# Kernel tuning notes

Hardware: AMD Instinct MI355X
Metric: run time of the kernel (lower is better)

## Reference

```python
import jax, jax.numpy as jnp
import numpy as np

B, T = 16, 512          # batch, timesteps
IN = 16                 # input_path_dim
D = 128                 # cde_state_dim
H = 256                 # vf_hidden_dim
L = 136                 # logsig_size = 16 + 16*15/2 (depth-2 log-signature)
O = 32                  # output_path_dim


def _linear_params(key, out_f, in_f):
    kw, kb = jax.random.split(key)
    lim = 1.0 / np.sqrt(in_f)
    W = jax.random.uniform(kw, (out_f, in_f), minval=-lim, maxval=lim, dtype=jnp.float32)
    b = jax.random.uniform(kb, (out_f,), minval=-lim, maxval=lim, dtype=jnp.float32)
    return W, b


def setup_inputs() -> dict:
    key = jax.random.key(0)
    ks = jax.random.split(key, 10)
    x0 = jax.random.normal(ks[0], (B, IN), dtype=jnp.float32)
    # log-signature increments are small; scale down for numerical realism
    logsigs = jax.random.normal(ks[1], (B, T - 1, L), dtype=jnp.float32) * 0.01
    # initial MLP: IN -> H -> H -> D (softplus activations, linear final)
    iw1, ib1 = _linear_params(ks[2], H, IN)
    iw2, ib2 = _linear_params(ks[3], H, H)
    iw3, ib3 = _linear_params(ks[4], D, H)
    # vector-field MLP: D -> H -> H -> D*L (softplus, tanh final)
    fw1, fb1 = _linear_params(ks[5], H, D)
    fw2, fb2 = _linear_params(ks[6], H, H)
    fw3, fb3 = _linear_params(ks[7], D * L, H)
    # readout: D -> O
    rw, rb = _linear_params(ks[8], O, D)
    return dict(x0=x0, logsigs=logsigs,
                iw1=iw1, ib1=ib1, iw2=iw2, ib2=ib2, iw3=iw3, ib3=ib3,
                fw1=fw1, fb1=fb1, fw2=fw2, fb2=fb2, fw3=fw3, fb3=fb3,
                rw=rw, rb=rb)


def reference(x0, logsigs, iw1, ib1, iw2, ib2, iw3, ib3,
              fw1, fb1, fw2, fb2, fw3, fb3, rw, rb):
    sp = jax.nn.softplus
    # initial MLP -> h0: (B, D)
    h0 = sp(x0 @ iw1.T + ib1)
    h0 = sp(h0 @ iw2.T + ib2)
    h0 = h0 @ iw3.T + ib3

    def step(h, logsig_t):
        # vector-field MLP: (B, D) -> (B, D*L), tanh final activation
        z = sp(h @ fw1.T + fb1)
        z = sp(z @ fw2.T + fb2)
        z = jnp.tanh(z @ fw3.T + fb3)
        mat = z.reshape(h.shape[0], D, L)          # (B, D, L)
        h_next = h + jnp.einsum('bdl,bl->bd', mat, logsig_t)
        return h_next, h_next

    # scan over time: xs shape (T-1, B, L)
    _, h_hist = jax.lax.scan(step, h0, jnp.swapaxes(logsigs, 0, 1))
    h_all = jnp.concatenate([h0[None, :, :], h_hist], axis=0)  # (T, B, D)
    out = h_all @ rw.T + rb                                     # (T, B, O)
    return jnp.swapaxes(out, 0, 1)                              # (B, T, O)
```

## Files before the change

kernel.cpp:

```cpp
#include <hip/hip_runtime.h>

namespace {
constexpr int kB = 16, kT = 512, kIN = 16, kD = 128, kH = 256, kL = 136, kO = 32;
constexpr int kSteps = kT - 1;
constexpr int NBLK = 256;
constexpr int NTHR = 512;
constexpr int NMLPB = 128;
constexpr int NT3 = 9;
constexpr int OFF_W3L = 0;
constexpr int OFF_Z2H = 73728;
constexpr int OFF_Z2L = 82432;
constexpr int OFF_OMS = 91136;
constexpr int OFF_RED = 100096;
constexpr size_t LDS_BYTES = 100608;
constexpr int OFF_FW2 = 0;
constexpr int OFF_Z1S = 33280;
constexpr int OFF_HB  = 34304;
constexpr int OFF_HHI = 34816;
constexpr int OFF_HLO = 35072;
}

typedef __attribute__((ext_vector_type(8))) _Float16 half8;
typedef __attribute__((ext_vector_type(4))) float f32x4;

__device__ __forceinline__ float softplusf(float x) {
  return fmaxf(x, 0.0f) + log1pf(expf(-fabsf(x)));
}
__device__ __forceinline__ unsigned short h2u(_Float16 h) {
  unsigned short u; __builtin_memcpy(&u, &h, 2); return u;
}
#define ALOAD64(p)    __hip_atomic_load((p),  __ATOMIC_RELAXED, __HIP_MEMORY_SCOPE_AGENT)
#define ASTORE64(p,v) __hip_atomic_store((p), (v), __ATOMIC_RELAXED, __HIP_MEMORY_SCOPE_AGENT)

__global__ void __launch_bounds__(256)
rde_init(const float* __restrict__ x0,
         const float* __restrict__ iw1, const float* __restrict__ ib1,
         const float* __restrict__ iw2, const float* __restrict__ ib2,
         const float* __restrict__ iw3, const float* __restrict__ ib3,
         float* __restrict__ hist) {
  __shared__ float xs[kIN];
  __shared__ __align__(16) float t1[kH];
  __shared__ __align__(16) float t2[kH];
  const int b = blockIdx.x, tid = threadIdx.x;
  if (tid < kIN) xs[tid] = x0[b*kIN + tid];
  __syncthreads();
  {
    float a = ib1[tid];
#pragma unroll
    for (int i = 0; i < kIN; ++i) a = fmaf(xs[i], iw1[tid*kIN + i], a);
    t1[tid] = softplusf(a);
  }
  __syncthreads();
  {
    const float4* wr = (const float4*)(iw2 + (size_t)tid*kH);
    float a = ib2[tid];
#pragma unroll 8
    for (int q = 0; q < kH/4; ++q) {
      float4 w = wr[q];
      a = fmaf(t1[4*q+0], w.x, a); a = fmaf(t1[4*q+1], w.y, a);
      a = fmaf(t1[4*q+2], w.z, a); a = fmaf(t1[4*q+3], w.w, a);
    }
    t2[tid] = softplusf(a);
  }
  __syncthreads();
  if (tid < kD) {
    const float4* wr = (const float4*)(iw3 + (size_t)tid*kH);
    float a = ib3[tid];
#pragma unroll 8
    for (int q = 0; q < kH/4; ++q) {
      float4 w = wr[q];
      a = fmaf(t2[4*q+0], w.x, a); a = fmaf(t2[4*q+1], w.y, a);
      a = fmaf(t2[4*q+2], w.z, a); a = fmaf(t2[4*q+3], w.w, a);
    }
    hist[(size_t)b*kD + tid] = a;
  }
}

__global__ void __launch_bounds__(NTHR, 1)
rde_scan(const float* __restrict__ lsg,
         const float* __restrict__ fw1, const float* __restrict__ fb1,
         const float* __restrict__ fw2, const float* __restrict__ fb2,
         const float* __restrict__ fw3, const float* __restrict__ fb3,
         float* __restrict__ hist,
         unsigned long long* z2x, unsigned long long* partx) {
  extern __shared__ char smem[];
  const int tid  = threadIdx.x;
  const int k    = blockIdx.x;
  const int wave = tid >> 6, lane = tid & 63;
  const int l15  = lane & 15, g = lane >> 4;

  if (k >= NMLPB) {
    _Float16* W3L  = (_Float16*)(smem + OFF_W3L);
    _Float16* z2hi = (_Float16*)(smem + OFF_Z2H);
    _Float16* z2lo = (_Float16*)(smem + OFF_Z2L);
    float* oms = (float*)(smem + OFF_OMS);
    float* red = (float*)(smem + OFF_RED);
    const int d_own = k - NMLPB;

    for (int i = tid; i < NT3*8*64; i += NTHR) {
      const int w = i >> 9, s = (i >> 6) & 7, ln = i & 63;
      const int nl = w*16 + (ln & 15), col = s*32 + (ln >> 4)*8;
      half8 hv;
      if (nl < kL) {
        const float* p = fw3 + ((size_t)d_own*kL + nl)*kH + col;
#pragma unroll
        for (int e = 0; e < 8; ++e) hv[e] = (_Float16)p[e];
      } else {
#pragma unroll
        for (int e = 0; e < 8; ++e) hv[e] = (_Float16)0.f;
      }
      *(half8*)(W3L + ((w*8 + s)*64 + ln)*8) = hv;
    }
    const float biasv = fb3[(size_t)d_own*kL + wave*16 + l15];
    const float bias8 = (wave == 7 && l15 < 8) ? fb3[(size_t)d_own*kL + 128 + l15] : 0.f;
    __syncthreads();

    for (int t = 0; t < kSteps; ++t) {
      const unsigned epw = (unsigned)(t + 1);
#pragma unroll 2
      for (int rep = 0; rep < 2; ++rep) {
        int cc = tid + rep*512;
        if (cc < 544) {
          int bb = cc / 34, ii = cc - bb*34;
          float4 v = *(const float4*)(lsg + ((size_t)bb*kSteps + t)*kL + ii*4);
          *(float4*)(oms + bb*140 + ii*4) = v;
        }
      }
      unsigned long long q8[8];
      {
        const unsigned long long* src = z2x + (size_t)tid*8;
        for (;;) {
          bool ok = true;
#pragma unroll
          for (int i = 0; i < 8; ++i) q8[i] = ALOAD64(src + i);
#pragma unroll
          for (int i = 0; i < 8; ++i) ok &= ((unsigned)(q8[i] >> 32) == epw);
          if (ok) break;
          __builtin_amdgcn_s_sleep(1);
        }
      }
      {
        const int e0 = tid*8, m = e0 >> 8, kk = e0 & 255;
        unsigned* ph = (unsigned*)(z2hi + m*272 + kk);
        unsigned* pl = (unsigned*)(z2lo + m*272 + kk);
#pragma unroll
        for (int i = 0; i < 4; ++i) {
          unsigned a = (unsigned)q8[2*i], b = (unsigned)q8[2*i+1];
          ph[i] = (a & 0xffffu) | (b << 16);
          pl[i] = (a >> 16) | (b & 0xffff0000u);
        }
      }
      __syncthreads();

      f32x4 acc = {biasv, biasv, biasv, biasv};
      f32x4 acc8 = {bias8, bias8, bias8, bias8};
#pragma unroll
      for (int s = 0; s < 8; ++s) {
        half8 ah = *(const half8*)(z2hi + l15*272 + s*32 + g*8);
        half8 al = *(const half8*)(z2lo + l15*272 + s*32 + g*8);
        half8 bh = *(const half8*)(W3L + ((wave*8 + s)*64 + lane)*8);
        acc = __builtin_amdgcn_mfma_f32_16x16x32_f16(ah, bh, acc, 0, 0, 0);
        acc = __builtin_amdgcn_mfma_f32_16x16x32_f16(al, bh, acc, 0, 0, 0);
        if (wave == 7) {
          half8 b8 = *(const half8*)(W3L + ((64 + s)*64 + lane)*8);
          acc8 = __builtin_amdgcn_mfma_f32_16x16x32_f16(ah, b8, acc8, 0, 0, 0);
          acc8 = __builtin_amdgcn_mfma_f32_16x16x32_f16(al, b8, acc8, 0, 0, 0);
        }
      }
#pragma unroll
      for (int r = 0; r < 4; ++r) {
        const int b = g*4 + r;
        float p = tanhf(acc[r]) * oms[b*140 + wave*16 + l15];
        if (wave == 7 && l15 < 8)
          p += tanhf(acc8[r]) * oms[b*140 + 128 + l15];
        p += __shfl_xor(p, 1); p += __shfl_xor(p, 2);
        p += __shfl_xor(p, 4); p += __shfl_xor(p, 8);
        if (l15 == 0) red[b*8 + wave] = p;
      }
      __syncthreads();
      if (tid < 16) {
        float s = 0.f;
#pragma unroll
        for (int w = 0; w < 8; ++w) s += red[tid*8 + w];
        unsigned long long pk = (unsigned long long)__float_as_uint(s)
                              | ((unsigned long long)epw << 32);
        ASTORE64(partx + (size_t)tid*NMLPB + d_own, pk);
      }
    }
  } else {
    float* fw2s = (float*)(smem + OFF_FW2);
    float* z1s  = (float*)(smem + OFF_Z1S);
    float* hb   = (float*)(smem + OFF_HB);
    _Float16* hhi = (_Float16*)(smem + OFF_HHI);
    _Float16* hlo = (_Float16*)(smem + OFF_HLO);
    const int b_own = k >> 3, e8 = k & 7, j0 = e8 * 32;

    half8 bw1[2][4];
    float fb1v[2];
#pragma unroll
    for (int ti = 0; ti < 2; ++ti) {
      const int n = (wave*2 + ti)*16 + l15;
      fb1v[ti] = fb1[n];
#pragma unroll
      for (int kst = 0; kst < 4; ++kst) {
        const float* p = fw1 + (size_t)n*kD + kst*32 + g*8;
        half8 h;
#pragma unroll
        for (int e = 0; e < 8; ++e) h[e] = (_Float16)p[e];
        bw1[ti][kst] = h;
      }
    }
    const float fb2v = fb2[j0 + (tid >> 4)];
    for (int i = tid; i < 32*64; i += NTHR) {
      int jl = i >> 6, q = i & 63;
      float4 v = *(const float4*)(fw2 + (size_t)(j0 + jl)*kH + q*4);
      *(float4*)(fw2s + jl*260 + q*4) = v;
    }
    if (tid < kD) {
      float hv = hist[(size_t)b_own*kD + tid];
      hb[tid] = hv;
      _Float16 hh = (_Float16)hv;
      hhi[tid] = hh; hlo[tid] = (_Float16)(hv - (float)hh);
    }
    __syncthreads();

    for (int t = 0; t < kSteps; ++t) {
      const unsigned epw = (unsigned)(t + 1);
      f32x4 a0 = {fb1v[0], fb1v[0], fb1v[0], fb1v[0]};
      f32x4 a1 = {fb1v[1], fb1v[1], fb1v[1], fb1v[1]};
#pragma unroll
      for (int kst = 0; kst < 4; ++kst) {
        half8 ah = *(const half8*)(hhi + kst*32 + g*8);
        half8 al = *(const half8*)(hlo + kst*32 + g*8);
        a0 = __builtin_amdgcn_mfma_f32_16x16x32_f16(ah, bw1[0][kst], a0, 0, 0, 0);
        a0 = __builtin_amdgcn_mfma_f32_16x16x32_f16(al, bw1[0][kst], a0, 0, 0, 0);
        a1 = __builtin_amdgcn_mfma_f32_16x16x32_f16(ah, bw1[1][kst], a1, 0, 0, 0);
        a1 = __builtin_amdgcn_mfma_f32_16x16x32_f16(al, bw1[1][kst], a1, 0, 0, 0);
      }
      if (g == 0) {
        z1s[(wave*2+0)*16 + l15] = softplusf(a0[0]);
        z1s[(wave*2+1)*16 + l15] = softplusf(a1[0]);
      }
      __syncthreads();
      {
        const int jl = tid >> 4, ks = tid & 15;
        float a = 0.f;
#pragma unroll
        for (int kh = ks; kh < kH; kh += 16)
          a = fmaf(z1s[kh], fw2s[jl*260 + kh], a);
        a += __shfl_xor(a, 1); a += __shfl_xor(a, 2);
        a += __shfl_xor(a, 4); a += __shfl_xor(a, 8);
        if (ks == 0) {
          float v = softplusf(a + fb2v);
          _Float16 vh = (_Float16)v;
          _Float16 vl = (_Float16)(v - (float)vh);
          unsigned long long pk =
              (unsigned long long)((unsigned)h2u(vh) | ((unsigned)h2u(vl) << 16))
            | ((unsigned long long)epw << 32);
          ASTORE64(z2x + b_own*kH + j0 + jl, pk);
        }
      }
      if (tid < kD) {
        const unsigned long long* pp = partx + (size_t)b_own*NMLPB + tid;
        unsigned long long q;
        for (;;) {
          q = ALOAD64(pp);
          if ((unsigned)(q >> 32) == epw) break;
          __builtin_amdgcn_s_sleep(1);
        }
        float hn = hb[tid] + __uint_as_float((unsigned)q);
        hb[tid] = hn;
        if (e8 == 0) hist[((size_t)(t+1)*kB + b_own)*kD + tid] = hn;
        _Float16 hh = (_Float16)hn;
        hhi[tid] = hh; hlo[tid] = (_Float16)(hn - (float)hh);
      }
      __syncthreads();
    }
  }
}

__global__ void __launch_bounds__(512)
rde_readout(const float* __restrict__ hist, const float* __restrict__ rw,
            const float* __restrict__ rb, float* __restrict__ out) {
  const int t = blockIdx.x, tid = threadIdx.x;
  const int b = tid >> 5, o = tid & 31;
  const float4* hr = (const float4*)(hist + ((size_t)t*kB + b)*kD);
  const float4* wr = (const float4*)(rw + (size_t)o*kD);
  float a = rb[o];
#pragma unroll 8
  for (int q = 0; q < kD/4; ++q) {
    float4 h4 = hr[q], w4 = wr[q];
    a = fmaf(h4.x,w4.x,a); a = fmaf(h4.y,w4.y,a);
    a = fmaf(h4.z,w4.z,a); a = fmaf(h4.w,w4.w,a);
  }
  out[((size_t)b*kT + t)*kO + o] = a;
}

extern "C" void kernel_launch(void* const* d_in, const int* in_sizes, int n_in,
                              void* d_out, int out_size, void* d_ws, size_t ws_size,
                              hipStream_t stream) {
  const float* x0  = (const float*)d_in[0];
  const float* lsg = (const float*)d_in[1];
  const float* iw1 = (const float*)d_in[2];
  const float* ib1 = (const float*)d_in[3];
  const float* iw2 = (const float*)d_in[4];
  const float* ib2 = (const float*)d_in[5];
  const float* iw3 = (const float*)d_in[6];
  const float* ib3 = (const float*)d_in[7];
  const float* fw1 = (const float*)d_in[8];
  const float* fb1 = (const float*)d_in[9];
  const float* fw2 = (const float*)d_in[10];
  const float* fb2 = (const float*)d_in[11];
  const float* fw3 = (const float*)d_in[12];
  const float* fb3 = (const float*)d_in[13];
  const float* rw  = (const float*)d_in[14];
  const float* rb  = (const float*)d_in[15];
  float* out = (float*)d_out;

  float* hist = (float*)d_ws;
  unsigned long long* z2x =
      (unsigned long long*)(hist + (size_t)kT*kB*kD);
  unsigned long long* partx = z2x + (size_t)kB*kH;

  hipMemsetAsync(z2x, 0, ((size_t)kB*kH + (size_t)kB*NMLPB)*8, stream);
  hipFuncSetAttribute((const void*)rde_scan,
                      hipFuncAttributeMaxDynamicSharedMemorySize, (int)LDS_BYTES);

  rde_init<<<kB, 256, 0, stream>>>(x0, iw1, ib1, iw2, ib2, iw3, ib3, hist);

  void* args[] = { (void*)&lsg, (void*)&fw1, (void*)&fb1, (void*)&fw2, (void*)&fb2,
                   (void*)&fw3, (void*)&fb3, (void*)&hist, (void*)&z2x, (void*)&partx };
  hipLaunchCooperativeKernel((const void*)rde_scan, dim3(NBLK), dim3(NTHR),
                             args, (unsigned)LDS_BYTES, stream);

  rde_readout<<<kT, 512, 0, stream>>>(hist, rw, rb, out);
}
```

Measured before the change: 4.840 ms.

## Replicate first two MLP layers in every block, drop producer-consumer split

The scan kernel drops its split into 128 MLP blocks and 128 fw3 blocks. Each of 128 blocks now recomputes layers 1 and 2 of the vector field for all 16 batches with MFMA, holding fw2 in registers. The only cross-block exchange per step is a single all-to-all of the partial h updates. This removes one of the two global handshakes per timestep and the z2 transfer, at the cost of redundant layer-1/2 compute and more registers per block. The launch also changes from a cooperative launch to a plain one, which drops the guarantee that all blocks are co-resident while the spin-wait still depends on it.

```diff
diff --git a/kernel.cpp b/kernel.cpp
--- a/kernel.cpp
+++ b/kernel.cpp
@@ -3,21 +3,19 @@
 namespace {
 constexpr int kB = 16, kT = 512, kIN = 16, kD = 128, kH = 256, kL = 136, kO = 32;
 constexpr int kSteps = kT - 1;
-constexpr int NBLK = 256;
+constexpr int NBLK = 128;
 constexpr int NTHR = 512;
-constexpr int NMLPB = 128;
-constexpr int NT3 = 9;
 constexpr int OFF_W3L = 0;
-constexpr int OFF_Z2H = 73728;
-constexpr int OFF_Z2L = 82432;
-constexpr int OFF_OMS = 91136;
-constexpr int OFF_RED = 100096;
-constexpr size_t LDS_BYTES = 100608;
-constexpr int OFF_FW2 = 0;
-constexpr int OFF_Z1S = 33280;
-constexpr int OFF_HB  = 34304;
-constexpr int OFF_HHI = 34816;
-constexpr int OFF_HLO = 35072;
+constexpr int OFF_Z1H = 73728;
+constexpr int OFF_Z1L = 82176;
+constexpr int OFF_Z2H = 90624;
+constexpr int OFF_Z2L = 99072;
+constexpr int OFF_HBH = 107520;
+constexpr int OFF_HBL = 111872;
+constexpr int OFF_HB  = 116224;
+constexpr int OFF_OMS = 124416;
+constexpr int OFF_RED = 133376;
+constexpr size_t LDS_BYTES = 133888;
 }
 
 typedef __attribute__((ext_vector_type(8))) _Float16 half8;
@@ -25,9 +23,6 @@
 
 __device__ __forceinline__ float softplusf(float x) {
   return fmaxf(x, 0.0f) + log1pf(expf(-fabsf(x)));
-}
-__device__ __forceinline__ unsigned short h2u(_Float16 h) {
-  unsigned short u; __builtin_memcpy(&u, &h, 2); return u;
 }
 #define ALOAD64(p)    __hip_atomic_load((p),  __ATOMIC_RELAXED, __HIP_MEMORY_SCOPE_AGENT)
 #define ASTORE64(p,v) __hip_atomic_store((p), (v), __ATOMIC_RELAXED, __HIP_MEMORY_SCOPE_AGENT)
@@ -76,206 +71,216 @@
   }
 }
 
-__global__ void __launch_bounds__(NTHR, 1)
+__global__ void __launch_bounds__(NTHR)
+__attribute__((amdgpu_waves_per_eu(1, 2)))
 rde_scan(const float* __restrict__ lsg,
          const float* __restrict__ fw1, const float* __restrict__ fb1,
          const float* __restrict__ fw2, const float* __restrict__ fb2,
          const float* __restrict__ fw3, const float* __restrict__ fb3,
-         float* __restrict__ hist,
-         unsigned long long* z2x, unsigned long long* partx) {
+         float* __restrict__ hist, unsigned long long* partx) {
   extern __shared__ char smem[];
+  _Float16* W3L  = (_Float16*)(smem + OFF_W3L);
+  _Float16* z1hi = (_Float16*)(smem + OFF_Z1H);
+  _Float16* z1lo = (_Float16*)(smem + OFF_Z1L);
+  _Float16* z2hi = (_Float16*)(smem + OFF_Z2H);
+  _Float16* z2lo = (_Float16*)(smem + OFF_Z2L);
+  _Float16* hbh  = (_Float16*)(smem + OFF_HBH);
+  _Float16* hbl  = (_Float16*)(smem + OFF_HBL);
+  float* hb  = (float*)(smem + OFF_HB);
+  float* oms = (float*)(smem + OFF_OMS);
+  float* red = (float*)(smem + OFF_RED);
+
   const int tid  = threadIdx.x;
-  const int k    = blockIdx.x;
+  const int d_own = blockIdx.x;
   const int wave = tid >> 6, lane = tid & 63;
   const int l15  = lane & 15, g = lane >> 4;
 
-  if (k >= NMLPB) {
-    _Float16* W3L  = (_Float16*)(smem + OFF_W3L);
-    _Float16* z2hi = (_Float16*)(smem + OFF_Z2H);
-    _Float16* z2lo = (_Float16*)(smem + OFF_Z2L);
-    float* oms = (float*)(smem + OFF_OMS);
-    float* red = (float*)(smem + OFF_RED);
-    const int d_own = k - NMLPB;
-
-    for (int i = tid; i < NT3*8*64; i += NTHR) {
-      const int w = i >> 9, s = (i >> 6) & 7, ln = i & 63;
-      const int nl = w*16 + (ln & 15), col = s*32 + (ln >> 4)*8;
-      half8 hv;
-      if (nl < kL) {
-        const float* p = fw3 + ((size_t)d_own*kL + nl)*kH + col;
-#pragma unroll
-        for (int e = 0; e < 8; ++e) hv[e] = (_Float16)p[e];
-      } else {
-#pragma unroll
-        for (int e = 0; e < 8; ++e) hv[e] = (_Float16)0.f;
-      }
-      *(half8*)(W3L + ((w*8 + s)*64 + ln)*8) = hv;
-    }
-    const float biasv = fb3[(size_t)d_own*kL + wave*16 + l15];
-    const float bias8 = (wave == 7 && l15 < 8) ? fb3[(size_t)d_own*kL + 128 + l15] : 0.f;
-    __syncthreads();
-
-    for (int t = 0; t < kSteps; ++t) {
-      const unsigned epw = (unsigned)(t + 1);
+  for (int i = tid; i < 9*8*64; i += NTHR) {
+    const int w = i >> 9, s = (i >> 6) & 7, ln = i & 63;
+    const int nl = w*16 + (ln & 15), col = s*32 + (ln >> 4)*8;
+    half8 hv;
+    if (nl < kL) {
+      const float* p = fw3 + ((size_t)d_own*kL + nl)*kH + col;
+#pragma unroll
+      for (int e = 0; e < 8; ++e) hv[e] = (_Float16)p[e];
+    } else {
+#pragma unroll
+      for (int e = 0; e < 8; ++e) hv[e] = (_Float16)0.f;
+    }
+    *(half8*)(W3L + ((w*8 + s)*64 + ln)*8) = hv;
+  }
+  const float biasv = fb3[(size_t)d_own*kL + wave*16 + l15];
+  const float bias8 = (wave == 7 && l15 < 8) ? fb3[(size_t)d_own*kL + 128 + l15] : 0.f;
+
+  half8 bw1[2][4];
+  float fb1v[2];
+#pragma unroll
+  for (int ti = 0; ti < 2; ++ti) {
+    const int n = (wave*2 + ti)*16 + l15;
+    fb1v[ti] = fb1[n];
+#pragma unroll
+    for (int kst = 0; kst < 4; ++kst) {
+      const float* p = fw1 + (size_t)n*kD + kst*32 + g*8;
+      half8 h;
+#pragma unroll
+      for (int e = 0; e < 8; ++e) h[e] = (_Float16)p[e];
+      bw1[ti][kst] = h;
+    }
+  }
+  half8 bw2[2][8];
+  float fb2v[2];
+#pragma unroll
+  for (int ti = 0; ti < 2; ++ti) {
+    const int n = (wave*2 + ti)*16 + l15;
+    fb2v[ti] = fb2[n];
+#pragma unroll
+    for (int kst = 0; kst < 8; ++kst) {
+      const float* p = fw2 + (size_t)n*kH + kst*32 + g*8;
+      half8 h;
+#pragma unroll
+      for (int e = 0; e < 8; ++e) h[e] = (_Float16)p[e];
+      bw2[ti][kst] = h;
+    }
+  }
+  {
+    const int idx = tid*4, b = idx >> 7, d = idx & 127;
+    float4 h4 = *(const float4*)(hist + (size_t)b*kD + d);
+    *(float4*)(hb + idx) = h4;
+    float hv[4] = {h4.x, h4.y, h4.z, h4.w};
+#pragma unroll
+    for (int i = 0; i < 4; ++i) {
+      _Float16 hh = (_Float16)hv[i];
+      hbh[b*136 + d + i] = hh;
+      hbl[b*136 + d + i] = (_Float16)(hv[i] - (float)hh);
+    }
+  }
+  __syncthreads();
+
+  for (int t = 0; t < kSteps; ++t) {
+    const unsigned epw = (unsigned)(t + 1);
+
 #pragma unroll 2
-      for (int rep = 0; rep < 2; ++rep) {
-        int cc = tid + rep*512;
-        if (cc < 544) {
-          int bb = cc / 34, ii = cc - bb*34;
-          float4 v = *(const float4*)(lsg + ((size_t)bb*kSteps + t)*kL + ii*4);
-          *(float4*)(oms + bb*140 + ii*4) = v;
-        }
-      }
-      unsigned long long q8[8];
-      {
-        const unsigned long long* src = z2x + (size_t)tid*8;
-        for (;;) {
-          bool ok = true;
-#pragma unroll
-          for (int i = 0; i < 8; ++i) q8[i] = ALOAD64(src + i);
-#pragma unroll
-          for (int i = 0; i < 8; ++i) ok &= ((unsigned)(q8[i] >> 32) == epw);
-          if (ok) break;
-          __builtin_amdgcn_s_sleep(1);
-        }
-      }
-      {
-        const int e0 = tid*8, m = e0 >> 8, kk = e0 & 255;
-        unsigned* ph = (unsigned*)(z2hi + m*272 + kk);
-        unsigned* pl = (unsigned*)(z2lo + m*272 + kk);
-#pragma unroll
-        for (int i = 0; i < 4; ++i) {
-          unsigned a = (unsigned)q8[2*i], b = (unsigned)q8[2*i+1];
-          ph[i] = (a & 0xffffu) | (b << 16);
-          pl[i] = (a >> 16) | (b & 0xffff0000u);
-        }
-      }
-      __syncthreads();
-
-      f32x4 acc = {biasv, biasv, biasv, biasv};
-      f32x4 acc8 = {bias8, bias8, bias8, bias8};
-#pragma unroll
-      for (int s = 0; s < 8; ++s) {
-        half8 ah = *(const half8*)(z2hi + l15*272 + s*32 + g*8);
-        half8 al = *(const half8*)(z2lo + l15*272 + s*32 + g*8);
-        half8 bh = *(const half8*)(W3L + ((wave*8 + s)*64 + lane)*8);
-        acc = __builtin_amdgcn_mfma_f32_16x16x32_f16(ah, bh, acc, 0, 0, 0);
-        acc = __builtin_amdgcn_mfma_f32_16x16x32_f16(al, bh, acc, 0, 0, 0);
-        if (wave == 7) {
-          half8 b8 = *(const half8*)(W3L + ((64 + s)*64 + lane)*8);
-          acc8 = __builtin_amdgcn_mfma_f32_16x16x32_f16(ah, b8, acc8, 0, 0, 0);
-          acc8 = __builtin_amdgcn_mfma_f32_16x16x32_f16(al, b8, acc8, 0, 0, 0);
-        }
-      }
-#pragma unroll
-      for (int r = 0; r < 4; ++r) {
-        const int b = g*4 + r;
-        float p = tanhf(acc[r]) * oms[b*140 + wave*16 + l15];
-        if (wave == 7 && l15 < 8)
-          p += tanhf(acc8[r]) * oms[b*140 + 128 + l15];
-        p += __shfl_xor(p, 1); p += __shfl_xor(p, 2);
-        p += __shfl_xor(p, 4); p += __shfl_xor(p, 8);
-        if (l15 == 0) red[b*8 + wave] = p;
-      }
-      __syncthreads();
-      if (tid < 16) {
-        float s = 0.f;
-#pragma unroll
-        for (int w = 0; w < 8; ++w) s += red[tid*8 + w];
-        unsigned long long pk = (unsigned long long)__float_as_uint(s)
-                              | ((unsigned long long)epw << 32);
-        ASTORE64(partx + (size_t)tid*NMLPB + d_own, pk);
-      }
-    }
-  } else {
-    float* fw2s = (float*)(smem + OFF_FW2);
-    float* z1s  = (float*)(smem + OFF_Z1S);
-    float* hb   = (float*)(smem + OFF_HB);
-    _Float16* hhi = (_Float16*)(smem + OFF_HHI);
-    _Float16* hlo = (_Float16*)(smem + OFF_HLO);
-    const int b_own = k >> 3, e8 = k & 7, j0 = e8 * 32;
-
-    half8 bw1[2][4];
-    float fb1v[2];
-#pragma unroll
-    for (int ti = 0; ti < 2; ++ti) {
-      const int n = (wave*2 + ti)*16 + l15;
-      fb1v[ti] = fb1[n];
-#pragma unroll
-      for (int kst = 0; kst < 4; ++kst) {
-        const float* p = fw1 + (size_t)n*kD + kst*32 + g*8;
-        half8 h;
-#pragma unroll
-        for (int e = 0; e < 8; ++e) h[e] = (_Float16)p[e];
-        bw1[ti][kst] = h;
-      }
-    }
-    const float fb2v = fb2[j0 + (tid >> 4)];
-    for (int i = tid; i < 32*64; i += NTHR) {
-      int jl = i >> 6, q = i & 63;
-      float4 v = *(const float4*)(fw2 + (size_t)(j0 + jl)*kH + q*4);
-      *(float4*)(fw2s + jl*260 + q*4) = v;
-    }
-    if (tid < kD) {
-      float hv = hist[(size_t)b_own*kD + tid];
-      hb[tid] = hv;
-      _Float16 hh = (_Float16)hv;
-      hhi[tid] = hh; hlo[tid] = (_Float16)(hv - (float)hh);
-    }
-    __syncthreads();
-
-    for (int t = 0; t < kSteps; ++t) {
-      const unsigned epw = (unsigned)(t + 1);
+    for (int rep = 0; rep < 2; ++rep) {
+      int cc = tid + rep*512;
+      if (cc < 544) {
+        int bb = cc / 34, ii = cc - bb*34;
+        float4 v = *(const float4*)(lsg + ((size_t)bb*kSteps + t)*kL + ii*4);
+        *(float4*)(oms + bb*140 + ii*4) = v;
+      }
+    }
+
+    {
       f32x4 a0 = {fb1v[0], fb1v[0], fb1v[0], fb1v[0]};
       f32x4 a1 = {fb1v[1], fb1v[1], fb1v[1], fb1v[1]};
 #pragma unroll
       for (int kst = 0; kst < 4; ++kst) {
-        half8 ah = *(const half8*)(hhi + kst*32 + g*8);
-        half8 al = *(const half8*)(hlo + kst*32 + g*8);
+        half8 ah = *(const half8*)(hbh + l15*136 + kst*32 + g*8);
+        half8 al = *(const half8*)(hbl + l15*136 + kst*32 + g*8);
         a0 = __builtin_amdgcn_mfma_f32_16x16x32_f16(ah, bw1[0][kst], a0, 0, 0, 0);
         a0 = __builtin_amdgcn_mfma_f32_16x16x32_f16(al, bw1[0][kst], a0, 0, 0, 0);
         a1 = __builtin_amdgcn_mfma_f32_16x16x32_f16(ah, bw1[1][kst], a1, 0, 0, 0);
         a1 = __builtin_amdgcn_mfma_f32_16x16x32_f16(al, bw1[1][kst], a1, 0, 0, 0);
       }
-      if (g == 0) {
-        z1s[(wave*2+0)*16 + l15] = softplusf(a0[0]);
-        z1s[(wave*2+1)*16 + l15] = softplusf(a1[0]);
-      }
-      __syncthreads();
-      {
-        const int jl = tid >> 4, ks = tid & 15;
-        float a = 0.f;
-#pragma unroll
-        for (int kh = ks; kh < kH; kh += 16)
-          a = fmaf(z1s[kh], fw2s[jl*260 + kh], a);
-        a += __shfl_xor(a, 1); a += __shfl_xor(a, 2);
-        a += __shfl_xor(a, 4); a += __shfl_xor(a, 8);
-        if (ks == 0) {
-          float v = softplusf(a + fb2v);
-          _Float16 vh = (_Float16)v;
-          _Float16 vl = (_Float16)(v - (float)vh);
-          unsigned long long pk =
-              (unsigned long long)((unsigned)h2u(vh) | ((unsigned)h2u(vl) << 16))
-            | ((unsigned long long)epw << 32);
-          ASTORE64(z2x + b_own*kH + j0 + jl, pk);
-        }
-      }
-      if (tid < kD) {
-        const unsigned long long* pp = partx + (size_t)b_own*NMLPB + tid;
-        unsigned long long q;
-        for (;;) {
-          q = ALOAD64(pp);
-          if ((unsigned)(q >> 32) == epw) break;
-          __builtin_amdgcn_s_sleep(1);
-        }
-        float hn = hb[tid] + __uint_as_float((unsigned)q);
-        hb[tid] = hn;
-        if (e8 == 0) hist[((size_t)(t+1)*kB + b_own)*kD + tid] = hn;
+#pragma unroll
+      for (int r = 0; r < 4; ++r) {
+        const int b = g*4 + r;
+        float v0 = softplusf(a0[r]);
+        float v1 = softplusf(a1[r]);
+        _Float16 h0 = (_Float16)v0, h1 = (_Float16)v1;
+        z1hi[b*264 + (wave*2+0)*16 + l15] = h0;
+        z1lo[b*264 + (wave*2+0)*16 + l15] = (_Float16)(v0 - (float)h0);
+        z1hi[b*264 + (wave*2+1)*16 + l15] = h1;
+        z1lo[b*264 + (wave*2+1)*16 + l15] = (_Float16)(v1 - (float)h1);
+      }
+    }
+    __syncthreads();
+
+    {
+      f32x4 a0 = {fb2v[0], fb2v[0], fb2v[0], fb2v[0]};
+      f32x4 a1 = {fb2v[1], fb2v[1], fb2v[1], fb2v[1]};
+#pragma unroll
+      for (int kst = 0; kst < 8; ++kst) {
+        half8 ah = *(const half8*)(z1hi + l15*264 + kst*32 + g*8);
+        half8 al = *(const half8*)(z1lo + l15*264 + kst*32 + g*8);
+        a0 = __builtin_amdgcn_mfma_f32_16x16x32_f16(ah, bw2[0][kst], a0, 0, 0, 0);
+        a0 = __builtin_amdgcn_mfma_f32_16x16x32_f16(al, bw2[0][kst], a0, 0, 0, 0);
+        a1 = __builtin_amdgcn_mfma_f32_16x16x32_f16(ah, bw2[1][kst], a1, 0, 0, 0);
+        a1 = __builtin_amdgcn_mfma_f32_16x16x32_f16(al, bw2[1][kst], a1, 0, 0, 0);
+      }
+#pragma unroll
+      for (int r = 0; r < 4; ++r) {
+        const int b = g*4 + r;
+        float v0 = softplusf(a0[r]);
+        float v1 = softplusf(a1[r]);
+        _Float16 h0 = (_Float16)v0, h1 = (_Float16)v1;
+        z2hi[b*264 + (wave*2+0)*16 + l15] = h0;
+        z2lo[b*264 + (wave*2+0)*16 + l15] = (_Float16)(v0 - (float)h0);
+        z2hi[b*264 + (wave*2+1)*16 + l15] = h1;
+        z2lo[b*264 + (wave*2+1)*16 + l15] = (_Float16)(v1 - (float)h1);
+      }
+    }
+    __syncthreads();
+
+    f32x4 acc = {biasv, biasv, biasv, biasv};
+    f32x4 acc8 = {bias8, bias8, bias8, bias8};
+#pragma unroll
+    for (int s = 0; s < 8; ++s) {
+      half8 ah = *(const half8*)(z2hi + l15*264 + s*32 + g*8);
+      half8 al = *(const half8*)(z2lo + l15*264 + s*32 + g*8);
+      half8 bh = *(const half8*)(W3L + ((wave*8 + s)*64 + lane)*8);
+      acc = __builtin_amdgcn_mfma_f32_16x16x32_f16(ah, bh, acc, 0, 0, 0);
+      acc = __builtin_amdgcn_mfma_f32_16x16x32_f16(al, bh, acc, 0, 0, 0);
+      if (wave == 7) {
+        half8 b8 = *(const half8*)(W3L + ((64 + s)*64 + lane)*8);
+        acc8 = __builtin_amdgcn_mfma_f32_16x16x32_f16(ah, b8, acc8, 0, 0, 0);
+        acc8 = __builtin_amdgcn_mfma_f32_16x16x32_f16(al, b8, acc8, 0, 0, 0);
+      }
+    }
+#pragma unroll
+    for (int r = 0; r < 4; ++r) {
+      const int b = g*4 + r;
+      float p = tanhf(acc[r]) * oms[b*140 + wave*16 + l15];
+      if (wave == 7 && l15 < 8)
+        p += tanhf(acc8[r]) * oms[b*140 + 128 + l15];
+      p += __shfl_xor(p, 1); p += __shfl_xor(p, 2);
+      p += __shfl_xor(p, 4); p += __shfl_xor(p, 8);
+      if (l15 == 0) red[b*8 + wave] = p;
+    }
+    __syncthreads();
+    if (tid < 16) {
+      float s = 0.f;
+#pragma unroll
+      for (int w = 0; w < 8; ++w) s += red[tid*8 + w];
+      unsigned long long pk = (unsigned long long)__float_as_uint(s)
+                            | ((unsigned long long)epw << 32);
+      ASTORE64(partx + (size_t)tid*NBLK + d_own, pk);
+    }
+
+    {
+      const unsigned long long* src = partx + (size_t)tid*4;
+      unsigned long long q4[4];
+      for (;;) {
+        bool ok = true;
+#pragma unroll
+        for (int i = 0; i < 4; ++i) q4[i] = ALOAD64(src + i);
+#pragma unroll
+        for (int i = 0; i < 4; ++i) ok &= ((unsigned)(q4[i] >> 32) == epw);
+        if (ok) break;
+        __builtin_amdgcn_s_sleep(1);
+      }
+      const int idx0 = tid*4, b = idx0 >> 7, d0 = idx0 & 127;
+#pragma unroll
+      for (int i = 0; i < 4; ++i) {
+        float hn = hb[idx0 + i] + __uint_as_float((unsigned)q4[i]);
+        hb[idx0 + i] = hn;
         _Float16 hh = (_Float16)hn;
-        hhi[tid] = hh; hlo[tid] = (_Float16)(hn - (float)hh);
-      }
-      __syncthreads();
-    }
+        hbh[b*136 + d0 + i] = hh;
+        hbl[b*136 + d0 + i] = (_Float16)(hn - (float)hh);
+      }
+    }
+    __syncthreads();
+    if (d_own < kB && tid < kD)
+      hist[((size_t)(t+1)*kB + d_own)*kD + tid] = hb[d_own*kD + tid];
   }
 }
 
@@ -318,20 +323,17 @@
   float* out = (float*)d_out;
 
   float* hist = (float*)d_ws;
-  unsigned long long* z2x =
+  unsigned long long* partx =
       (unsigned long long*)(hist + (size_t)kT*kB*kD);
-  unsigned long long* partx = z2x + (size_t)kB*kH;
-
-  hipMemsetAsync(z2x, 0, ((size_t)kB*kH + (size_t)kB*NMLPB)*8, stream);
+
+  hipMemsetAsync(partx, 0, (size_t)kB*NBLK*8, stream);
   hipFuncSetAttribute((const void*)rde_scan,
                       hipFuncAttributeMaxDynamicSharedMemorySize, (int)LDS_BYTES);
 
   rde_init<<<kB, 256, 0, stream>>>(x0, iw1, ib1, iw2, ib2, iw3, ib3, hist);
 
-  void* args[] = { (void*)&lsg, (void*)&fw1, (void*)&fb1, (void*)&fw2, (void*)&fb2,
-                   (void*)&fw3, (void*)&fb3, (void*)&hist, (void*)&z2x, (void*)&partx };
-  hipLaunchCooperativeKernel((const void*)rde_scan, dim3(NBLK), dim3(NTHR),
-                             args, (unsigned)LDS_BYTES, stream);
+  rde_scan<<<NBLK, NTHR, LDS_BYTES, stream>>>(
+      lsg, fw1, fb1, fw2, fb2, fw3, fb3, hist, partx);
 
   rde_readout<<<kT, 512, 0, stream>>>(hist, rw, rb, out);
 }
```

Result: slower. 7.740 ms (+59.9%).
